# Kernel tuning notes

Measured on AMD Instinct MI355X. Metric: run time of the kernel, lower is better.

## Reference

```python
import jax, jax.numpy as jnp
import numpy as np

IN_C, OUT_C, MAX_SIZE = 512, 256, 256
N = MAX_SIZE * MAX_SIZE  # 65536 nodes
E = MAX_SIZE * MAX_SIZE  # 65536 edges (before self loops)
NEG_SLOPE = 0.2


def setup_inputs() -> dict:
    key = jax.random.key(0)
    ks = jax.random.split(key, 12)
    s = 1.0 / np.sqrt(IN_C)
    so = 1.0 / np.sqrt(OUT_C)
    return {
        "x": jax.random.normal(ks[0], (N, IN_C), dtype=jnp.float32),
        "x_mask": jnp.ones((N,), dtype=bool),
        "edge_index": jax.random.randint(ks[1], (2, E), 0, N),
        "edge_mask": jnp.ones((E,), dtype=bool),
        "vaild_mask": jnp.ones((MAX_SIZE, MAX_SIZE), dtype=bool),
        # self-loop Linear
        "W_self": jax.random.uniform(ks[2], (IN_C, OUT_C), jnp.float32, -s, s),
        "b_self": jax.random.uniform(ks[3], (OUT_C,), jnp.float32, -s, s),
        # GATv2Conv params (heads=1)
        "W_l": jax.random.uniform(ks[4], (IN_C, OUT_C), jnp.float32, -s, s),
        "b_l": jnp.zeros((OUT_C,), jnp.float32),
        "W_r": jax.random.uniform(ks[5], (IN_C, OUT_C), jnp.float32, -s, s),
        "b_r": jnp.zeros((OUT_C,), jnp.float32),
        "att": jax.random.uniform(ks[6], (OUT_C,), jnp.float32, -so, so),
        "conv_bias": jnp.zeros((OUT_C,), jnp.float32),
        # sk classifier (out_channels -> 1)
        "W_cls": jax.random.uniform(ks[7], (OUT_C, 1), jnp.float32, -so, so),
        "b_cls": jax.random.uniform(ks[8], (1,), jnp.float32, -so, so),
    }


def _forward(x, edge_index, W_self, b_self, W_l, b_l, W_r, b_r, att,
             conv_bias, W_cls, b_cls):
    n = x.shape[0]
    # PyG GATv2Conv adds self-loops by default
    loops = jnp.arange(n, dtype=edge_index.dtype)
    src = jnp.concatenate([edge_index[0], loops])
    dst = jnp.concatenate([edge_index[1], loops])

    x_l = x @ W_l + b_l  # source-side transform (n, out)
    x_r = x @ W_r + b_r  # target-side transform (n, out)

    # per-edge GATv2 attention logits
    h = jax.nn.leaky_relu(x_l[src] + x_r[dst], NEG_SLOPE)  # (Etot, out)
    e = h @ att  # (Etot,)

    # segment softmax over incoming edges of each target node
    m = jnp.full((n,), -jnp.inf, dtype=e.dtype).at[dst].max(e)
    p = jnp.exp(e - m[dst])
    denom = jax.ops.segment_sum(p, dst, num_segments=n)
    alpha = p / denom[dst]

    x_neigh = jax.ops.segment_sum(alpha[:, None] * x_l[src], dst,
                                  num_segments=n) + conv_bias
    x_out = (x @ W_self + b_self) + x_neigh

    # sinkhorn-style row softmax channel (sk_channel=1, n1=n2=max_size)
    ms = MAX_SIZE
    sk = (x_out @ W_cls + b_cls).reshape(ms, ms)
    sk = jax.nn.softmax(sk, axis=-1)
    x_out = x_out + sk.reshape(-1, 1)
    # n1*n2 == max_size**2, so the padded output equals x_out
    return x_out


def reference(x, x_mask, edge_index, edge_mask, vaild_mask, W_self, b_self,
              W_l, b_l, W_r, b_r, att, conv_bias, W_cls, b_cls):
    # masks are all-True (fully valid case): x_valid = x, edges all kept
    return _forward(x, edge_index, W_self, b_self, W_l, b_l, W_r, b_r, att,
                    conv_bias, W_cls, b_cls)
```

## Files before the change

kernel.cpp:

```cpp
#include <hip/hip_runtime.h>
#include <hip/hip_bf16.h>
#include <stdint.h>

#define NNODE 65536
#define NEDGE 65536
#define ETOT  (NNODE + NEDGE)
#define INC   512
#define OUTC  256
#define NEG_SLOPE 0.2f
#define SLOTCAP 32

typedef __attribute__((ext_vector_type(8))) __bf16 bf16x8;
typedef __attribute__((ext_vector_type(4))) float f32x4;

__device__ __forceinline__ float b2f(unsigned short u) {
  return __uint_as_float(((unsigned int)u) << 16);
}
__device__ __forceinline__ unsigned short f2b(float f) {
  unsigned int u = __float_as_uint(f);
  u += 0x7fffu + ((u >> 16) & 1u);
  return (unsigned short)(u >> 16);
}
__device__ __forceinline__ unsigned int pk2(float lo, float hi) {
  return (unsigned int)f2b(lo) | ((unsigned int)f2b(hi) << 16);
}
__device__ __forceinline__ float lrelu(float v) {
  return v > 0.f ? v : NEG_SLOPE * v;
}

__global__ __launch_bounds__(256) void cvt_x_kernel(const float* __restrict__ x,
                                                    unsigned short* __restrict__ xb) {
  size_t i = ((size_t)blockIdx.x * 256 + threadIdx.x) * 4;
  float4 v = *(const float4*)(x + i);
  ushort4 o = { f2b(v.x), f2b(v.y), f2b(v.z), f2b(v.w) };
  *(ushort4*)(xb + i) = o;
}

__global__ __launch_bounds__(256) void prep_w_kernel(
    const float* __restrict__ Wl, const float* __restrict__ Wr, const float* __restrict__ Ws,
    const float* __restrict__ bl, const float* __restrict__ br, const float* __restrict__ bs,
    unsigned short* __restrict__ WT, float* __restrict__ bcat) {
  int i = blockIdx.x * 256 + threadIdx.x;
  if (i < 768 * 512) {
    int o = i >> 9, k = i & 511;
    float v;
    if (o < 256)      v = Wl[k * 256 + o];
    else if (o < 512) v = Wr[k * 256 + (o - 256)];
    else              v = Ws[k * 256 + (o - 512)];
    WT[i] = f2b(v);
  }
  if (i < 768) {
    bcat[i] = (i < 256) ? bl[i] : (i < 512 ? br[i - 256] : bs[i - 512]);
  }
}

__global__ __launch_bounds__(512) void gemm_kernel(
    const unsigned short* __restrict__ Xb,
    const unsigned short* __restrict__ WT,
    const float* __restrict__ bcat,
    unsigned short* __restrict__ xl,
    unsigned short* __restrict__ xr,
    unsigned short* __restrict__ xs) {
  __shared__ __align__(16) char smem[131072];
  unsigned short* sm = (unsigned short*)smem;

  const int wid = blockIdx.x;
  const int xcd = wid & 7;
  const int local = wid >> 3;
  const int by = local % 3;
  const int rowt = xcd * 32 + local / 3;
  const int rowBase = rowt * 256;
  const int colBase = by * 256;

  const int tid = threadIdx.x;
  const int lane = tid & 63;
  const int w = tid >> 6;
  const int wm = (w >> 2) * 128;
  const int wn = (w & 3) * 64;

  f32x4 acc[8][4] = {};

  auto stage = [&](int kk, int buf) {
    const int q = tid;
    const int slot_sw = q & 7;
#pragma unroll
    for (int l = 0; l < 4; ++l) {
      const int r = l * 64 + (q >> 3);
      const int slot = slot_sw ^ (r & 7);
      const unsigned short* gA = Xb + (size_t)(rowBase + r) * 512 + kk + slot * 8;
      __builtin_amdgcn_global_load_lds(
          (const __attribute__((address_space(1))) void*)gA,
          (__attribute__((address_space(3))) void*)(sm + buf * 32768 + l * 4096 + q * 8), 16, 0, 0);
      const unsigned short* gB = WT + (size_t)(colBase + r) * 512 + kk + slot * 8;
      __builtin_amdgcn_global_load_lds(
          (const __attribute__((address_space(1))) void*)gB,
          (__attribute__((address_space(3))) void*)(sm + buf * 32768 + 16384 + l * 4096 + q * 8), 16, 0, 0);
    }
  };

#define COMPUTE(bufidx) { \
    const unsigned short* As = sm + (bufidx) * 32768; \
    const unsigned short* Bs = As + 16384; \
    _Pragma("unroll") \
    for (int kh = 0; kh < 2; ++kh) { \
      bf16x8 bfr[4]; \
      _Pragma("unroll") \
      for (int n = 0; n < 4; ++n) { \
        const int rB = wn + n * 16 + (lane & 15); \
        const int sB = (kh * 4 + (lane >> 4)) ^ (rB & 7); \
        bfr[n] = *(const bf16x8*)&Bs[rB * 64 + sB * 8]; \
      } \
      _Pragma("unroll") \
      for (int m = 0; m < 8; ++m) { \
        const int rA = wm + m * 16 + (lane & 15); \
        const int sA = (kh * 4 + (lane >> 4)) ^ (rA & 7); \
        bf16x8 afr = *(const bf16x8*)&As[rA * 64 + sA * 8]; \
        __builtin_amdgcn_s_setprio(1); \
        _Pragma("unroll") \
        for (int n = 0; n < 4; ++n) \
          acc[m][n] = __builtin_amdgcn_mfma_f32_16x16x32_bf16(afr, bfr[n], acc[m][n], 0, 0, 0); \
        __builtin_amdgcn_s_setprio(0); \
      } \
    } \
  }

  stage(0, 0);
  stage(64, 1);
  asm volatile("s_waitcnt vmcnt(8)" ::: "memory");
  __builtin_amdgcn_s_barrier();

  for (int t = 0; t < 8; ++t) {
    const int buf = t & 1;
    __builtin_amdgcn_sched_barrier(0);
    COMPUTE(buf);
    __builtin_amdgcn_sched_barrier(0);
    __builtin_amdgcn_s_barrier();
    if (t + 2 < 8) {
      stage((t + 2) * 64, buf);
      asm volatile("s_waitcnt vmcnt(8)" ::: "memory");
    } else {
      asm volatile("s_waitcnt vmcnt(0)" ::: "memory");
    }
    __builtin_amdgcn_s_barrier();
  }
#undef COMPUTE

  {
    unsigned short* dst = (by == 0) ? xl : (by == 1) ? xr : xs;
    float* eps = (float*)smem + w * 1088;
    float biasn[4];
#pragma unroll
    for (int n = 0; n < 4; ++n) biasn[n] = bcat[colBase + wn + n * 16 + (lane & 15)];
#pragma unroll
    for (int m = 0; m < 8; ++m) {
#pragma unroll
      for (int n = 0; n < 4; ++n)
#pragma unroll
        for (int j = 0; j < 4; ++j)
          eps[((lane >> 4) * 4 + j) * 68 + n * 16 + (lane & 15)] = acc[m][n][j] + biasn[n];
#pragma unroll
      for (int it = 0; it < 2; ++it) {
        const int r16 = it * 8 + (lane >> 3);
        const int c8 = (lane & 7) * 8;
        const float* srcp = eps + r16 * 68 + c8;
        float4 v0 = *(const float4*)srcp;
        float4 v1 = *(const float4*)(srcp + 4);
        uint4 o;
        o.x = pk2(v0.x, v0.y);
        o.y = pk2(v0.z, v0.w);
        o.z = pk2(v1.x, v1.y);
        o.w = pk2(v1.z, v1.w);
        *(uint4*)(dst + (size_t)(rowBase + wm + m * 16 + r16) * 256 + wn + c8) = o;
      }
    }
  }
}

__global__ __launch_bounds__(256) void edge_logit_kernel(
    const int* __restrict__ ei,
    const unsigned short* __restrict__ xl,
    const unsigned short* __restrict__ xr,
    const float* __restrict__ att,
    int* __restrict__ cnt,
    int* __restrict__ slot_src,
    float* __restrict__ slot_e) {
  const int j = blockIdx.x * 8 + (threadIdx.x >> 5);
  const int lane = threadIdx.x & 31;
  int src, dst;
  if (j < NEDGE) { src = ei[j]; dst = ei[NEDGE + j]; }
  else           { src = j - NEDGE; dst = src; }
  const int c = lane * 8;
  uint4 ul = *(const uint4*)(xl + (size_t)src * 256 + c);
  uint4 ur = *(const uint4*)(xr + (size_t)dst * 256 + c);
  float4 a0 = *(const float4*)(att + c);
  float4 a1 = *(const float4*)(att + c + 4);
  float s = lrelu(b2f((unsigned short)ul.x) + b2f((unsigned short)ur.x)) * a0.x
          + lrelu(b2f((unsigned short)(ul.x >> 16)) + b2f((unsigned short)(ur.x >> 16))) * a0.y
          + lrelu(b2f((unsigned short)ul.y) + b2f((unsigned short)ur.y)) * a0.z
          + lrelu(b2f((unsigned short)(ul.y >> 16)) + b2f((unsigned short)(ur.y >> 16))) * a0.w
          + lrelu(b2f((unsigned short)ul.z) + b2f((unsigned short)ur.z)) * a1.x
          + lrelu(b2f((unsigned short)(ul.z >> 16)) + b2f((unsigned short)(ur.z >> 16))) * a1.y
          + lrelu(b2f((unsigned short)ul.w) + b2f((unsigned short)ur.w)) * a1.z
          + lrelu(b2f((unsigned short)(ul.w >> 16)) + b2f((unsigned short)(ur.w >> 16))) * a1.w;
#pragma unroll
  for (int off = 16; off; off >>= 1) s += __shfl_xor(s, off);
  if (lane == 0) {
    const int pos = atomicAdd(&cnt[dst], 1);
    if (pos < SLOTCAP) {
      slot_src[dst * SLOTCAP + pos] = src;
      slot_e[dst * SLOTCAP + pos] = s;
    }
  }
}

__global__ __launch_bounds__(256) void node_kernel(
    const int* __restrict__ cnt,
    const int* __restrict__ slot_src, const float* __restrict__ slot_e,
    const unsigned short* __restrict__ xl,
    const unsigned short* __restrict__ xs,
    const float* __restrict__ conv_bias,
    float* __restrict__ out,
    const float* __restrict__ Wcls, const float* __restrict__ bcls,
    float* __restrict__ logits) {
  const int n = blockIdx.x * 4 + (threadIdx.x >> 6);
  const int lane = threadIdx.x & 63;
  const int base = n * SLOTCAP;
  const int deg = cnt[n];

  float m = -1e30f;
  for (int k = 0; k < deg; ++k) m = fmaxf(m, slot_e[base + k]);
  float denom = 0.f;
  for (int k = 0; k < deg; ++k) denom += __expf(slot_e[base + k] - m);
  const float inv = 1.f / denom;

  const int c = lane * 4;
  float4 accv = {0.f, 0.f, 0.f, 0.f};
  for (int k = 0; k < deg; ++k) {
    const float alpha = __expf(slot_e[base + k] - m) * inv;
    const int src = slot_src[base + k];
    ushort4 u = *(const ushort4*)(xl + (size_t)src * 256 + c);
    accv.x += alpha * b2f(u.x);
    accv.y += alpha * b2f(u.y);
    accv.z += alpha * b2f(u.z);
    accv.w += alpha * b2f(u.w);
  }
  ushort4 s4 = *(const ushort4*)(xs + (size_t)n * 256 + c);
  float4 cb = *(const float4*)(conv_bias + c);
  float4 cur;
  cur.x = b2f(s4.x) + accv.x + cb.x;
  cur.y = b2f(s4.y) + accv.y + cb.y;
  cur.z = b2f(s4.z) + accv.z + cb.z;
  cur.w = b2f(s4.w) + accv.w + cb.w;
  const size_t o = (size_t)n * 256 + c;
  *(float4*)(out + o) = cur;

  float4 wc = *(const float4*)(Wcls + c);
  float part = cur.x * wc.x + cur.y * wc.y + cur.z * wc.z + cur.w * wc.w;
#pragma unroll
  for (int off = 32; off; off >>= 1) part += __shfl_xor(part, off, 64);
  if (lane == 0) logits[n] = part + bcls[0];
}

__global__ __launch_bounds__(256) void sk_kernel(const float* __restrict__ logits,
                                                 float* __restrict__ out) {
  __shared__ float sv[256];
  __shared__ float red[256];
  const int r = blockIdx.x >> 2;
  const int q = blockIdx.x & 3;
  const int t = threadIdx.x;
  const float v = logits[r * 256 + t];
  red[t] = v;
  __syncthreads();
  for (int d = 128; d; d >>= 1) {
    if (t < d) red[t] = fmaxf(red[t], red[t + d]);
    __syncthreads();
  }
  const float mx = red[0];
  __syncthreads();
  const float p = __expf(v - mx);
  red[t] = p;
  __syncthreads();
  for (int d = 128; d; d >>= 1) {
    if (t < d) red[t] += red[t + d];
    __syncthreads();
  }
  const float sum = red[0];
  sv[t] = p / sum;
  __syncthreads();
  const size_t rowbase = (size_t)r * 256 * 256;
  for (int i = q * 64; i < q * 64 + 64; ++i) {
    out[rowbase + (size_t)i * 256 + t] += sv[i];
  }
}

extern "C" void kernel_launch(void* const* d_in, const int* in_sizes, int n_in,
                              void* d_out, int out_size, void* d_ws, size_t ws_size,
                              hipStream_t stream) {
  const float* x        = (const float*)d_in[0];
  const int*   ei       = (const int*)d_in[2];
  const float* W_self   = (const float*)d_in[5];
  const float* b_self   = (const float*)d_in[6];
  const float* W_l      = (const float*)d_in[7];
  const float* b_l      = (const float*)d_in[8];
  const float* W_r      = (const float*)d_in[9];
  const float* b_r      = (const float*)d_in[10];
  const float* att      = (const float*)d_in[11];
  const float* conv_bias= (const float*)d_in[12];
  const float* W_cls    = (const float*)d_in[13];
  const float* b_cls    = (const float*)d_in[14];
  float* out = (float*)d_out;

  char* ws = (char*)d_ws;
  size_t off = 0;
  auto alloc = [&](size_t bytes) {
    char* p = ws + off;
    off += (bytes + 255) & ~(size_t)255;
    return p;
  };
  unsigned short* xb   = (unsigned short*)alloc((size_t)NNODE * INC * 2);
  unsigned short* WT   = (unsigned short*)alloc((size_t)768 * 512 * 2);
  float*          bcat = (float*)alloc(768 * 4);
  unsigned short* xlb  = (unsigned short*)alloc((size_t)NNODE * OUTC * 2);
  unsigned short* xrb  = (unsigned short*)alloc((size_t)NNODE * OUTC * 2);
  unsigned short* xsb  = (unsigned short*)alloc((size_t)NNODE * OUTC * 2);
  int*            cnt  = (int*)alloc((size_t)NNODE * 4);
  float*          logits  = (float*)alloc((size_t)NNODE * 4);
  int*   slot_src = (int*)xb;
  float* slot_e   = (float*)(xb + (size_t)NNODE * SLOTCAP * 2);
  (void)ws_size; (void)in_sizes; (void)n_in; (void)out_size;

  hipMemsetAsync(cnt, 0, (size_t)NNODE * 4, stream);

  cvt_x_kernel<<<(NNODE * INC) / (256 * 4), 256, 0, stream>>>(x, xb);
  prep_w_kernel<<<(768 * 512 + 255) / 256, 256, 0, stream>>>(W_l, W_r, W_self, b_l, b_r, b_self, WT, bcat);
  gemm_kernel<<<768, 512, 0, stream>>>(xb, WT, bcat, xlb, xrb, xsb);
  edge_logit_kernel<<<ETOT / 8, 256, 0, stream>>>(ei, xlb, xrb, att, cnt, slot_src, slot_e);
  node_kernel<<<NNODE / 4, 256, 0, stream>>>(cnt, slot_src, slot_e, xlb, xsb, conv_bias,
                                             out, W_cls, b_cls, logits);
  sk_kernel<<<1024, 256, 0, stream>>>(logits, out);
}
```

Before: 205.4 us.

## Restructure GEMM mainloop into 4-stage K=32 pipeline with register double-buffered fragments

```diff
diff --git a/kernel.cpp b/kernel.cpp
--- a/kernel.cpp
+++ b/kernel.cpp
@@ -30,10 +30,15 @@
 
 __global__ __launch_bounds__(256) void cvt_x_kernel(const float* __restrict__ x,
                                                     unsigned short* __restrict__ xb) {
-  size_t i = ((size_t)blockIdx.x * 256 + threadIdx.x) * 4;
-  float4 v = *(const float4*)(x + i);
-  ushort4 o = { f2b(v.x), f2b(v.y), f2b(v.z), f2b(v.w) };
-  *(ushort4*)(xb + i) = o;
+  size_t i = ((size_t)blockIdx.x * 256 + threadIdx.x) * 8;
+  float4 v0 = *(const float4*)(x + i);
+  float4 v1 = *(const float4*)(x + i + 4);
+  uint4 o;
+  o.x = pk2(v0.x, v0.y);
+  o.y = pk2(v0.z, v0.w);
+  o.z = pk2(v1.x, v1.y);
+  o.w = pk2(v1.z, v1.w);
+  *(uint4*)(xb + i) = o;
 }
 
 __global__ __launch_bounds__(256) void prep_w_kernel(
@@ -80,70 +85,79 @@
 
   f32x4 acc[8][4] = {};
 
-  auto stage = [&](int kk, int buf) {
+  auto stage = [&](int t, int buf) {
+    const int kk = t * 32;
     const int q = tid;
-    const int slot_sw = q & 7;
-#pragma unroll
-    for (int l = 0; l < 4; ++l) {
-      const int r = l * 64 + (q >> 3);
-      const int slot = slot_sw ^ (r & 7);
+    const int sl = q & 3;
+#pragma unroll
+    for (int l = 0; l < 2; ++l) {
+      const int r = l * 128 + (q >> 2);
+      const int slot = sl ^ ((r >> 1) & 3);
       const unsigned short* gA = Xb + (size_t)(rowBase + r) * 512 + kk + slot * 8;
       __builtin_amdgcn_global_load_lds(
           (const __attribute__((address_space(1))) void*)gA,
-          (__attribute__((address_space(3))) void*)(sm + buf * 32768 + l * 4096 + q * 8), 16, 0, 0);
+          (__attribute__((address_space(3))) void*)(sm + buf * 16384 + l * 4096 + q * 8), 16, 0, 0);
       const unsigned short* gB = WT + (size_t)(colBase + r) * 512 + kk + slot * 8;
       __builtin_amdgcn_global_load_lds(
           (const __attribute__((address_space(1))) void*)gB,
-          (__attribute__((address_space(3))) void*)(sm + buf * 32768 + 16384 + l * 4096 + q * 8), 16, 0, 0);
+          (__attribute__((address_space(3))) void*)(sm + buf * 16384 + 8192 + l * 4096 + q * 8), 16, 0, 0);
     }
   };
 
-#define COMPUTE(bufidx) { \
-    const unsigned short* As = sm + (bufidx) * 32768; \
-    const unsigned short* Bs = As + 16384; \
+  auto ldfrag = [&](int buf, bf16x8* fa, bf16x8* fb) {
+    const unsigned short* As = sm + buf * 16384;
+    const unsigned short* Bs = As + 8192;
+    const int kq = lane >> 4;
+#pragma unroll
+    for (int m = 0; m < 8; ++m) {
+      const int rA = wm + m * 16 + (lane & 15);
+      fa[m] = *(const bf16x8*)&As[rA * 32 + ((kq ^ ((rA >> 1) & 3)) << 3)];
+    }
+#pragma unroll
+    for (int n = 0; n < 4; ++n) {
+      const int rB = wn + n * 16 + (lane & 15);
+      fb[n] = *(const bf16x8*)&Bs[rB * 32 + ((kq ^ ((rB >> 1) & 3)) << 3)];
+    }
+  };
+
+#define MFMA_BLOCK(FA, FB) { \
+    __builtin_amdgcn_s_setprio(1); \
     _Pragma("unroll") \
-    for (int kh = 0; kh < 2; ++kh) { \
-      bf16x8 bfr[4]; \
+    for (int m = 0; m < 8; ++m) \
       _Pragma("unroll") \
-      for (int n = 0; n < 4; ++n) { \
-        const int rB = wn + n * 16 + (lane & 15); \
-        const int sB = (kh * 4 + (lane >> 4)) ^ (rB & 7); \
-        bfr[n] = *(const bf16x8*)&Bs[rB * 64 + sB * 8]; \
-      } \
-      _Pragma("unroll") \
-      for (int m = 0; m < 8; ++m) { \
-        const int rA = wm + m * 16 + (lane & 15); \
-        const int sA = (kh * 4 + (lane >> 4)) ^ (rA & 7); \
-        bf16x8 afr = *(const bf16x8*)&As[rA * 64 + sA * 8]; \
-        __builtin_amdgcn_s_setprio(1); \
-        _Pragma("unroll") \
-        for (int n = 0; n < 4; ++n) \
-          acc[m][n] = __builtin_amdgcn_mfma_f32_16x16x32_bf16(afr, bfr[n], acc[m][n], 0, 0, 0); \
-        __builtin_amdgcn_s_setprio(0); \
-      } \
-    } \
-  }
+      for (int n = 0; n < 4; ++n) \
+        acc[m][n] = __builtin_amdgcn_mfma_f32_16x16x32_bf16((FA)[m], (FB)[n], acc[m][n], 0, 0, 0); \
+    __builtin_amdgcn_s_setprio(0); \
+  }
+
+  bf16x8 fa0[8], fb0[4], fa1[8], fb1[4];
 
   stage(0, 0);
-  stage(64, 1);
+  stage(1, 1);
+  stage(2, 2);
   asm volatile("s_waitcnt vmcnt(8)" ::: "memory");
   __builtin_amdgcn_s_barrier();
-
-  for (int t = 0; t < 8; ++t) {
-    const int buf = t & 1;
-    __builtin_amdgcn_sched_barrier(0);
-    COMPUTE(buf);
-    __builtin_amdgcn_sched_barrier(0);
-    __builtin_amdgcn_s_barrier();
-    if (t + 2 < 8) {
-      stage((t + 2) * 64, buf);
-      asm volatile("s_waitcnt vmcnt(8)" ::: "memory");
+  __builtin_amdgcn_sched_barrier(0);
+  ldfrag(0, fa0, fb0);
+
+#pragma unroll
+  for (int t = 0; t < 16; ++t) {
+    if (t <= 13)      asm volatile("s_waitcnt vmcnt(4)" ::: "memory");
+    else if (t == 14) asm volatile("s_waitcnt vmcnt(0)" ::: "memory");
+    if (t < 15) {
+      __builtin_amdgcn_s_barrier();
+      __builtin_amdgcn_sched_barrier(0);
+    }
+    if (t + 3 < 16) stage(t + 3, (t + 3) & 3);
+    if ((t & 1) == 0) {
+      if (t + 1 < 16) ldfrag((t + 1) & 3, fa1, fb1);
+      MFMA_BLOCK(fa0, fb0);
     } else {
-      asm volatile("s_waitcnt vmcnt(0)" ::: "memory");
-    }
-    __builtin_amdgcn_s_barrier();
-  }
-#undef COMPUTE
+      if (t + 1 < 16) ldfrag((t + 1) & 3, fa0, fb0);
+      MFMA_BLOCK(fa1, fb1);
+    }
+  }
+#undef MFMA_BLOCK
 
   {
     unsigned short* dst = (by == 0) ? xl : (by == 1) ? xr : xs;
@@ -331,7 +345,7 @@
 
   hipMemsetAsync(cnt, 0, (size_t)NNODE * 4, stream);
 
-  cvt_x_kernel<<<(NNODE * INC) / (256 * 4), 256, 0, stream>>>(x, xb);
+  cvt_x_kernel<<<(NNODE * INC) / (256 * 8), 256, 0, stream>>>(x, xb);
   prep_w_kernel<<<(768 * 512 + 255) / 256, 256, 0, stream>>>(W_l, W_r, W_self, b_l, b_r, b_self, WT, bcat);
   gemm_kernel<<<768, 512, 0, stream>>>(xb, WT, bcat, xlb, xrb, xsb);
   edge_logit_kernel<<<ETOT / 8, 256, 0, stream>>>(ei, xlb, xrb, att, cnt, slot_src, slot_e);
```

After: 209.4 us. No clear change (+2.0%).
